# Kernel optimization log

Hardware: AMD Instinct MI355X
Metric: run time of the kernel (lower is better)

## Reference

```python
import jax, jax.numpy as jnp
import numpy as np

CS = 64          # chunk_size
CP = CS - 1      # causal_padding
H = 8            # heads
DH = 64          # dim_head
SCALE = DH ** -0.5


def rotate_half(x):
    x1, x2 = jnp.split(x, 2, axis=-1)
    return jnp.concatenate((-x2, x1), axis=-1)


def apply_rope(t, freqs):
    rd = freqs.shape[-1]
    t_rot, t_pass = t[..., :rd], t[..., rd:]
    t_rot = t_rot * jnp.cos(freqs) + rotate_half(t_rot) * jnp.sin(freqs)
    return jnp.concatenate((t_rot, t_pass), axis=-1)


def setup_inputs() -> dict:
    key = jax.random.key(0)
    ks = jax.random.split(key, 10)
    b, n, dim = 4, 4096, 1024
    k_chunks, r, rlen = 64, 2, 128
    inner = H * DH
    return {
        "x": jax.random.normal(ks[0], (b, n, dim), dtype=jnp.float32),
        "context": jax.random.normal(ks[1], (b, k_chunks, r, rlen, dim), dtype=jnp.float32),
        "q_pos_emb": jax.random.normal(ks[2], (1, 1, CS, DH), dtype=jnp.float32),
        "k_pos_emb": jax.random.normal(ks[3], (1, 1, rlen, DH), dtype=jnp.float32),
        "Wq": jax.random.normal(ks[4], (dim, inner), dtype=jnp.float32) * 0.02,
        "Wk": jax.random.normal(ks[5], (dim, inner), dtype=jnp.float32) * 0.02,
        "Wv": jax.random.normal(ks[6], (dim, inner), dtype=jnp.float32) * 0.02,
        "Wo": jax.random.normal(ks[7], (inner, dim), dtype=jnp.float32) * 0.02,
        "bo": jnp.zeros((dim,), dtype=jnp.float32),
        "null_k": jax.random.normal(ks[8], (inner,), dtype=jnp.float32),
        "null_v": jax.random.normal(ks[9], (inner,), dtype=jnp.float32),
    }


def reference(x, context, q_pos_emb, k_pos_emb, Wq, Wk, Wv, Wo, bo, null_k, null_v):
    b, n, dim = x.shape
    _, k_chunks, r, rlen, _ = context.shape
    # causal shift: drop first CP tokens, pad CP zeros at end (F.pad with -CP)
    xs = jnp.pad(x[:, CP:], ((0, 0), (0, CP), (0, 0)))
    seq_index = (n // CS) * CS
    rem = n - seq_index
    xs = xs[:, :seq_index]                                   # [b, k*CS, dim]
    # shift q rope the same way; pad region gets freqs=0 -> identity rotation
    qpe = jnp.pad(q_pos_emb[:, :, CP:], ((0, 0), (0, 0), (0, CP), (0, 0)))
    kpe = jnp.tile(k_pos_emb, (1, 1, r, 1))                  # [1,1,r*rlen,DH]
    bk = b * k_chunks
    xc = xs.reshape(bk, CS, dim)
    ctx = context.reshape(bk, r * rlen, dim)
    # projections -> [bk, h, seq, dh]
    q = (xc @ Wq).reshape(bk, CS, H, DH).transpose(0, 2, 1, 3) * SCALE
    k = (ctx @ Wk).reshape(bk, r * rlen, H, DH).transpose(0, 2, 1, 3)
    v = (ctx @ Wv).reshape(bk, r * rlen, H, DH).transpose(0, 2, 1, 3)
    q = apply_rope(q, qpe)
    k = apply_rope(k, kpe)
    # null kv prepend
    nk = jnp.broadcast_to(null_k.reshape(1, H, 1, DH), (bk, H, 1, DH))
    nv = jnp.broadcast_to(null_v.reshape(1, H, 1, DH), (bk, H, 1, DH))
    k = jnp.concatenate((nk, k), axis=2)
    v = jnp.concatenate((nv, v), axis=2)
    sim = jnp.einsum('bhid,bhjd->bhij', q, k)
    attn = jax.nn.softmax(sim, axis=-1)
    o = jnp.einsum('bhij,bhjd->bhid', attn, v)
    o = o.transpose(0, 2, 1, 3).reshape(bk, CS, H * DH)
    o = o @ Wo + bo                                          # [bk, CS, dim]
    o = o.reshape(b, k_chunks * CS, dim)
    # unshift: pad CP zeros at front, trim CP - rem from end
    o = jnp.concatenate(
        (jnp.zeros((b, CP, dim), o.dtype), o[:, :k_chunks * CS - CP + rem]), axis=1)
    return o
```

## Files before the change

### kernel.cpp

```cpp
#include <hip/hip_runtime.h>


#define DEV __device__ __forceinline__

typedef __bf16 bf16x8 __attribute__((ext_vector_type(8)));
typedef float f32x4 __attribute__((ext_vector_type(4)));

DEV unsigned short f2bf(float f) {
  union { float f; unsigned int u; } v; v.f = f;
  unsigned int u = v.u;
  unsigned int r = (u + 0x7FFFu + ((u >> 16) & 1u)) >> 16;
  return (unsigned short)r;
}
DEV float bf2f(unsigned short h) {
  union { unsigned int u; float f; } v; v.u = ((unsigned int)h) << 16;
  return v.f;
}
DEV unsigned int pkbf(unsigned int hi, unsigned int lo) {
  return __builtin_amdgcn_perm(hi, lo, 0x07060302u);
}

DEV void ldst16(const void* g, void* l) {
  __builtin_amdgcn_global_load_lds(
      (const __attribute__((address_space(1))) void*)g,
      (__attribute__((address_space(3))) void*)l, 16, 0, 0);
}

DEV void bar() { __builtin_amdgcn_s_barrier(); }
#define LGKM0 asm volatile("s_waitcnt lgkmcnt(0)" ::: "memory")
#define VMCNT4 asm volatile("s_waitcnt vmcnt(4)" ::: "memory")
#define VMCNT0 asm volatile("s_waitcnt vmcnt(0)" ::: "memory")

__global__ __launch_bounds__(256) void prep_k(const float* __restrict__ Wq,
                                              const float* __restrict__ Wk,
                                              const float* __restrict__ Wv,
                                              const float* __restrict__ Wo,
                                              const float* __restrict__ qpe,
                                              const float* __restrict__ kpe,
                                              unsigned short* __restrict__ Wqt,
                                              unsigned short* __restrict__ Wkt,
                                              unsigned short* __restrict__ Wvt,
                                              unsigned short* __restrict__ Wot,
                                              float* __restrict__ ck, float* __restrict__ sk,
                                              float* __restrict__ cq, float* __restrict__ sq,
                                              float* __restrict__ out) {
  __shared__ float tl[64][65];
  int blk = blockIdx.x;
  int tid = threadIdx.x;
  if (blk < 512) {
    int mat = blk >> 7, loc = blk & 127;
    const float* W;
    unsigned short* Wt;
    int R, C;
    float scale = 1.0f;
    if (mat == 0)      { W = Wq; Wt = Wqt; R = 1024; C = 512; scale = 0.125f; }
    else if (mat == 1) { W = Wk; Wt = Wkt; R = 1024; C = 512; }
    else if (mat == 2) { W = Wv; Wt = Wvt; R = 1024; C = 512; }
    else               { W = Wo; Wt = Wot; R = 512;  C = 1024; }
    int nct = C >> 6;
    int rt = loc / nct, ct = loc % nct;
    int r0 = rt << 6, c0 = ct << 6;
    #pragma unroll
    for (int i = 0; i < 16; ++i) {
      int flat = i * 256 + tid;
      int rr = flat >> 6, cc = flat & 63;
      tl[rr][cc] = W[(size_t)(r0 + rr) * C + c0 + cc] * scale;
    }
    __syncthreads();
    #pragma unroll
    for (int i = 0; i < 16; ++i) {
      int flat = i * 256 + tid;
      int cc = flat >> 6, rr = flat & 63;
      Wt[(size_t)(c0 + cc) * R + r0 + rr] = f2bf(tl[rr][cc]);
    }
  } else if (blk < 764) {
    int r = blk - 512;
    int b = r / 63, rr = r % 63;
    float4 z = {0.f, 0.f, 0.f, 0.f};
    *(float4*)(out + (((size_t)(b * 4096 + rr)) << 10) + tid * 4) = z;
  } else {
    int t = (blk - 764) * 256 + tid;
    float f = kpe[t];
    ck[t] = cosf(f);
    sk[t] = sinf(f);
    if (t < 64) {
      float g = qpe[63 * 64 + t];
      cq[t] = cosf(g);
      sq[t] = sinf(g);
    }
  }
}

template <int MODE>
__global__ __launch_bounds__(256) void gemm_proj(const float* __restrict__ Af,
                                                 const unsigned short* __restrict__ B0,
                                                 const unsigned short* __restrict__ B1,
                                                 unsigned short* __restrict__ out0,
                                                 unsigned short* __restrict__ out1,
                                                 const float* __restrict__ ck,
                                                 const float* __restrict__ sk,
                                                 const float* __restrict__ cq,
                                                 const float* __restrict__ sq) {
  __shared__ unsigned short sh[16384];
  unsigned short* As = sh;
  unsigned short* Bs = sh + 8192;
  const int K = 1024;

  int id = blockIdx.x;
  int x, y, z;
  if (MODE == 0) { x = (id & 7) + 8 * (id >> 5); y = (id >> 3) & 3; z = 0; }
  else           { x = (id & 7) + 8 * (id >> 6); int j = (id >> 3) & 7; y = j & 3; z = j >> 2; }
  const unsigned short* B = z ? B1 : B0;
  int m0 = x * 128, n0 = y * 128;
  int tid = threadIdx.x, w = tid >> 6, lane = tid & 63;
  int wm = (w & 1) * 64, wn = (w >> 1) * 64;
  int Lrow = lane >> 3, Lc = lane & 7;
  int srcC = Lc ^ (Lrow & 7);

  const float* asrc[4];
  bool avalid[4];
  #pragma unroll
  for (int q = 0; q < 4; ++q) {
    int t = w * 4 + q;
    int gm = m0 + t * 8 + Lrow;
    if (MODE == 0) {
      int b = gm >> 12, p = gm & 4095;
      avalid[q] = (p <= 4032);
      asrc[q] = Af + (((size_t)(b << 12) + p + 63) << 10) + srcC * 8;
    } else {
      avalid[q] = true;
      asrc[q] = Af + (size_t)gm * 1024 + srcC * 8;
    }
  }

  f32x4 acc[4][4] = {};

  for (int k0 = 0; k0 < K; k0 += 64) {
    #pragma unroll
    for (int q = 0; q < 4; ++q) {
      int t = w * 4 + q;
      uint4 lo = {0, 0, 0, 0}, hi = {0, 0, 0, 0};
      if (avalid[q]) {
        lo = *(const uint4*)(asrc[q] + k0);
        hi = *(const uint4*)(asrc[q] + k0 + 4);
      }
      uint4 pk;
      pk.x = pkbf(lo.y, lo.x);
      pk.y = pkbf(lo.w, lo.z);
      pk.z = pkbf(hi.y, hi.x);
      pk.w = pkbf(hi.w, hi.z);
      *(uint4*)((char*)As + t * 1024 + lane * 16) = pk;
      ldst16(B + (size_t)(n0 + t * 8 + Lrow) * K + (k0 + srcC * 8), (char*)Bs + t * 1024);
    }
    __syncthreads();
    #pragma unroll
    for (int k32 = 0; k32 < 2; ++k32) {
      int c = k32 * 4 + (lane >> 4);
      bf16x8 af[4], bfr[4];
      #pragma unroll
      for (int mt = 0; mt < 4; ++mt) {
        int m = wm + mt * 16 + (lane & 15);
        af[mt] = *(const bf16x8*)((const char*)As + m * 128 + (c ^ (m & 7)) * 16);
      }
      #pragma unroll
      for (int nt = 0; nt < 4; ++nt) {
        int n = wn + nt * 16 + (lane & 15);
        bfr[nt] = *(const bf16x8*)((const char*)Bs + n * 128 + (c ^ (n & 7)) * 16);
      }
      #pragma unroll
      for (int mt = 0; mt < 4; ++mt)
        #pragma unroll
        for (int nt = 0; nt < 4; ++nt)
          acc[mt][nt] = __builtin_amdgcn_mfma_f32_16x16x32_bf16(af[mt], bfr[nt], acc[mt][nt], 0, 0, 0);
    }
    __syncthreads();
  }

  if (MODE == 0) {
    #pragma unroll
    for (int mt = 0; mt < 4; ++mt)
      #pragma unroll
      for (int nt = 0; nt < 4; ++nt)
        #pragma unroll
        for (int r = 0; r < 4; ++r) {
          int m = m0 + wm + mt * 16 + (lane >> 4) * 4 + r;
          int n = n0 + wn + nt * 16 + (lane & 15);
          float val = acc[mt][nt][r];
          if ((m & 63) == 0) {
            int d = nt * 16 + (lane & 15);
            float partner = acc[mt][nt ^ 2][r];
            val = val * cq[d] + (nt < 2 ? -partner : partner) * sq[d];
          }
          out0[(size_t)m * 512 + n] = f2bf(val);
        }
  } else if (z == 0) {
    #pragma unroll
    for (int mt = 0; mt < 4; ++mt)
      #pragma unroll
      for (int r = 0; r < 4; ++r) {
        int m = m0 + wm + mt * 16 + (lane >> 4) * 4 + r;
        int fib = (m & 127) * 64;
        #pragma unroll
        for (int nt = 0; nt < 4; ++nt) {
          int n = n0 + wn + nt * 16 + (lane & 15);
          int d = nt * 16 + (lane & 15);
          float partner = acc[mt][nt ^ 2][r];
          float val = acc[mt][nt][r] * ck[fib + d] + (nt < 2 ? -partner : partner) * sk[fib + d];
          out0[(size_t)m * 512 + n] = f2bf(val);
        }
      }
  } else {
    #pragma unroll
    for (int mt = 0; mt < 4; ++mt)
      #pragma unroll
      for (int nt = 0; nt < 4; ++nt)
        #pragma unroll
        for (int r = 0; r < 4; ++r) {
          int ml = wm + mt * 16 + (lane >> 4) * 4 + r;
          int nl = wn + nt * 16 + (lane & 15);
          int mc = ml >> 3, me = ml & 7;
          *(unsigned short*)((char*)sh + nl * 256 + ((mc ^ (nl & 15)) * 16) + me * 2) =
              f2bf(acc[mt][nt][r]);
        }
    __syncthreads();
    #pragma unroll
    for (int i = 0; i < 8; ++i) {
      int flat = i * 256 + tid;
      int nl = flat >> 4, mc = flat & 15;
      uint4 v = *(const uint4*)((const char*)sh + nl * 256 + ((mc ^ (nl & 15)) * 16));
      *(uint4*)(out1 + (size_t)(n0 + nl) * 65536 + m0 + mc * 8) = v;
    }
  }
}

DEV bf16x8 rdfrag(const unsigned short* b, int row, int c) {
  return *(const bf16x8*)((const char*)b + row * 128 + ((c ^ (row & 7)) << 4));
}

DEV void rdA(const unsigned short* bufA, int wm, int ln15, int l4, int mtb,
             bf16x8 (&af)[2][2]) {
  #pragma unroll
  for (int mq = 0; mq < 2; ++mq)
    #pragma unroll
    for (int kk = 0; kk < 2; ++kk)
      af[mq][kk] = rdfrag(bufA, wm + (mtb + mq) * 16 + ln15, kk * 4 + l4);
}

DEV void rdB(const unsigned short* bufB, int wn, int ln15, int l4, bf16x8 (&bf)[4][2]) {
  #pragma unroll
  for (int nt = 0; nt < 4; ++nt)
    #pragma unroll
    for (int kk = 0; kk < 2; ++kk)
      bf[nt][kk] = rdfrag(bufB, wn + nt * 16 + ln15, kk * 4 + l4);
}

template <int MTB>
DEV void mfma16(const bf16x8 (&af)[2][2], const bf16x8 (&bf)[4][2], f32x4 (&acc)[8][4]) {
  __builtin_amdgcn_s_setprio(1);
  #pragma unroll
  for (int mq = 0; mq < 2; ++mq)
    #pragma unroll
    for (int nt = 0; nt < 4; ++nt)
      #pragma unroll
      for (int kk = 0; kk < 2; ++kk)
        acc[MTB + mq][nt] = __builtin_amdgcn_mfma_f32_16x16x32_bf16(
            af[mq][kk], bf[nt][kk], acc[MTB + mq][nt], 0, 0, 0);
  __builtin_amdgcn_s_setprio(0);
}

DEV void aload(const float* Af, int m0, int rowt, int csrc, int k0, uint4 (&al)[8]) {
  #pragma unroll
  for (int q = 0; q < 4; ++q) {
    const float* s = Af + (size_t)(m0 + q * 64 + rowt) * 1024 + k0 + csrc * 8;
    al[2 * q] = *(const uint4*)s;
    al[2 * q + 1] = *(const uint4*)(s + 4);
  }
}

DEV void apack(unsigned short* bufA, int tid, const uint4 (&al)[8]) {
  #pragma unroll
  for (int q = 0; q < 4; ++q) {
    uint4 pk;
    pk.x = pkbf(al[2 * q].y, al[2 * q].x);
    pk.y = pkbf(al[2 * q].w, al[2 * q].z);
    pk.z = pkbf(al[2 * q + 1].y, al[2 * q + 1].x);
    pk.w = pkbf(al[2 * q + 1].w, al[2 * q + 1].z);
    *(uint4*)((char*)bufA + ((q * 512 + tid) << 4)) = pk;
  }
}

DEV void bstage(unsigned short* bufB, const unsigned short* Bsrc, int n0, int w,
                int Lrow, int srcC, int k0, int h) {
  #pragma unroll
  for (int qq = 0; qq < 2; ++qq) {
    int q = 2 * h + qq;
    ldst16(Bsrc + (size_t)(n0 + q * 64 + w * 8 + Lrow) * 1024 + k0 + srcC * 8,
           (char*)bufB + ((q * 512 + w * 64) << 4));
  }
}

__global__ __launch_bounds__(512, 2) void gemm_kv(const float* __restrict__ Af,
                                                  const unsigned short* __restrict__ Bk,
                                                  const unsigned short* __restrict__ Bv,
                                                  unsigned short* __restrict__ kb,
                                                  unsigned short* __restrict__ vtg,
                                                  const float* __restrict__ ck,
                                                  const float* __restrict__ sk) {
  __shared__ unsigned short sh[65536];
  unsigned short* A0b = sh;
  unsigned short* A1b = sh + 16384;
  unsigned short* B0b = sh + 32768;
  unsigned short* B1b = sh + 49152;

  int id = blockIdx.x;
  int x = (id & 7) + 8 * (id >> 5);
  int j = (id >> 3) & 3;
  int y = j & 1, z = j >> 1;
  const unsigned short* Bz = z ? Bv : Bk;
  int m0 = x << 8, n0 = y << 8;

  int tid = threadIdx.x, w = tid >> 6, lane = tid & 63;
  int wm = (w & 1) * 128, wn = (w >> 1) * 64;
  int ln15 = lane & 15, l4 = lane >> 4;
  int Lrow = lane >> 3;
  int srcC = (lane & 7) ^ (Lrow & 7);
  int rowt = tid >> 3;
  int csrc = (tid & 7) ^ (rowt & 7);

  f32x4 acc[8][4] = {};
  uint4 al[8];

  aload(Af, m0, rowt, csrc, 0, al);
  bstage(B0b, Bz, n0, w, Lrow, srcC, 0, 0);
  bstage(B0b, Bz, n0, w, Lrow, srcC, 0, 1);
  bstage(B1b, Bz, n0, w, Lrow, srcC, 64, 0);
  bstage(B1b, Bz, n0, w, Lrow, srcC, 64, 1);
  apack(A0b, tid, al);
  LGKM0;
  VMCNT4;
  bar();

  for (int it = 0; it < 8; ++it) {
    const int k0a = it * 128;
    bf16x8 af[2][2], bf[4][2];

    rdB(B0b, wn, ln15, l4, bf);
    rdA(A0b, wm, ln15, l4, 0, af);
    aload(Af, m0, rowt, csrc, k0a + 64, al);
    bar();
    mfma16<0>(af, bf, acc);
    bar();

    rdA(A0b, wm, ln15, l4, 2, af);
    bar();
    mfma16<2>(af, bf, acc);
    bar();

    rdA(A0b, wm, ln15, l4, 4, af);
    bstage(B0b, Bz, n0, w, Lrow, srcC, (k0a + 128) & 1023, 0);
    bar();
    mfma16<4>(af, bf, acc);
    bar();

    rdA(A0b, wm, ln15, l4, 6, af);
    bstage(B0b, Bz, n0, w, Lrow, srcC, (k0a + 128) & 1023, 1);
    apack(A1b, tid, al);
    LGKM0;
    VMCNT4;
    bar();
    mfma16<6>(af, bf, acc);
    bar();

    rdB(B1b, wn, ln15, l4, bf);
    rdA(A1b, wm, ln15, l4, 0, af);
    aload(Af, m0, rowt, csrc, (k0a + 128) & 1023, al);
    bar();
    mfma16<0>(af, bf, acc);
    bar();

    rdA(A1b, wm, ln15, l4, 2, af);
    bar();
    mfma16<2>(af, bf, acc);
    bar();

    rdA(A1b, wm, ln15, l4, 4, af);
    bstage(B1b, Bz, n0, w, Lrow, srcC, (k0a + 192) & 1023, 0);
    bar();
    mfma16<4>(af, bf, acc);
    bar();

    rdA(A1b, wm, ln15, l4, 6, af);
    bstage(B1b, Bz, n0, w, Lrow, srcC, (k0a + 192) & 1023, 1);
    apack(A0b, tid, al);
    LGKM0;
    VMCNT4;
    bar();
    mfma16<6>(af, bf, acc);
    bar();
  }

  VMCNT0;
  bar();

  if (z == 0) {
    #pragma unroll
    for (int mt = 0; mt < 8; ++mt)
      #pragma unroll
      for (int r = 0; r < 4; ++r) {
        int m = m0 + wm + mt * 16 + l4 * 4 + r;
        int fib = (m & 127) << 6;
        #pragma unroll
        for (int nt = 0; nt < 4; ++nt) {
          int d = nt * 16 + ln15;
          float partner = acc[mt][nt ^ 2][r];
          float val = acc[mt][nt][r] * ck[fib + d] + (nt < 2 ? -partner : partner) * sk[fib + d];
          kb[(size_t)m * 512 + n0 + wn + d] = f2bf(val);
        }
      }
  } else {
    #pragma unroll
    for (int mt = 0; mt < 8; ++mt)
      #pragma unroll
      for (int nt = 0; nt < 4; ++nt)
        #pragma unroll
        for (int r = 0; r < 4; ++r) {
          int ml = wm + mt * 16 + l4 * 4 + r;
          int nl = wn + nt * 16 + ln15;
          int mc = ml >> 3, me = ml & 7;
          *(unsigned short*)((char*)sh + nl * 512 + ((mc ^ (nl & 31)) << 4) + me * 2) =
              f2bf(acc[mt][nt][r]);
        }
    __syncthreads();
    #pragma unroll
    for (int i = 0; i < 16; ++i) {
      int flat = i * 512 + tid;
      int nl = flat >> 5, mc = flat & 31;
      uint4 v = *(const uint4*)((const char*)sh + nl * 512 + ((mc ^ (nl & 31)) << 4));
      *(uint4*)(vtg + (size_t)(n0 + nl) * 65536 + m0 + mc * 8) = v;
    }
  }
}

__global__ __launch_bounds__(256) void gemm_out(const unsigned short* __restrict__ A,
                                                const unsigned short* __restrict__ B,
                                                const float* __restrict__ bias,
                                                float* __restrict__ out) {
  __shared__ unsigned short sh[16384];
  unsigned short* As = sh;
  unsigned short* Bs = sh + 8192;
  const int K = 512, N = 1024;
  int id = blockIdx.x;
  int x = (id & 7) + 8 * (id >> 6), y = (id >> 3) & 7;
  int m0 = x * 128, n0 = y * 128;
  int tid = threadIdx.x, w = tid >> 6, lane = tid & 63;
  int wm = (w & 1) * 64, wn = (w >> 1) * 64;
  int Lrow = lane >> 3, Lc = lane & 7;
  int srcC = Lc ^ (Lrow & 7);

  f32x4 acc[4][4] = {};

  for (int k0 = 0; k0 < K; k0 += 64) {
    #pragma unroll
    for (int q = 0; q < 4; ++q) {
      int t = w * 4 + q;
      ldst16(A + (size_t)(m0 + t * 8 + Lrow) * K + (k0 + srcC * 8), (char*)As + t * 1024);
      ldst16(B + (size_t)(n0 + t * 8 + Lrow) * K + (k0 + srcC * 8), (char*)Bs + t * 1024);
    }
    __syncthreads();
    #pragma unroll
    for (int k32 = 0; k32 < 2; ++k32) {
      int c = k32 * 4 + (lane >> 4);
      bf16x8 af[4], bfr[4];
      #pragma unroll
      for (int mt = 0; mt < 4; ++mt) {
        int m = wm + mt * 16 + (lane & 15);
        af[mt] = *(const bf16x8*)((const char*)As + m * 128 + (c ^ (m & 7)) * 16);
      }
      #pragma unroll
      for (int nt = 0; nt < 4; ++nt) {
        int n = wn + nt * 16 + (lane & 15);
        bfr[nt] = *(const bf16x8*)((const char*)Bs + n * 128 + (c ^ (n & 7)) * 16);
      }
      #pragma unroll
      for (int mt = 0; mt < 4; ++mt)
        #pragma unroll
        for (int nt = 0; nt < 4; ++nt)
          acc[mt][nt] = __builtin_amdgcn_mfma_f32_16x16x32_bf16(af[mt], bfr[nt], acc[mt][nt], 0, 0, 0);
    }
    __syncthreads();
  }
  #pragma unroll
  for (int mt = 0; mt < 4; ++mt)
    #pragma unroll
    for (int nt = 0; nt < 4; ++nt)
      #pragma unroll
      for (int r = 0; r < 4; ++r) {
        int m = m0 + wm + mt * 16 + (lane >> 4) * 4 + r;
        int n = n0 + wn + nt * 16 + (lane & 15);
        int b = m >> 12, t = m & 4095;
        if (t <= 4032)
          out[((size_t)((b << 12) + t + 63)) * N + n] = acc[mt][nt][r] + bias[n];
      }
}

__global__ __launch_bounds__(256) void attn_kernel(const unsigned short* __restrict__ qb,
                                                   const unsigned short* __restrict__ kb,
                                                   const unsigned short* __restrict__ vtg,
                                                   const float* __restrict__ nullk,
                                                   const float* __restrict__ nullv,
                                                   unsigned short* __restrict__ ob) {
  __shared__ unsigned short qs[64 * 64];
  __shared__ unsigned short ks[256 * 64];
  __shared__ unsigned short ps[64 * 256];
  __shared__ float rnull[64];
  __shared__ float rsum[64];
  int id = blockIdx.x;
  int bc = (id & 7) + 8 * (id >> 6);
  int h = (id >> 3) & 7;
  int tid = threadIdx.x, w = tid >> 6, lane = tid & 63;
  int Lrow = lane >> 3, Lc = lane & 7, srcC = Lc ^ (Lrow & 7);

  #pragma unroll
  for (int q8 = 0; q8 < 2; ++q8) {
    int t = w * 2 + q8;
    ldst16(qb + (size_t)(bc * 64 + t * 8 + Lrow) * 512 + h * 64 + srcC * 8, (char*)qs + t * 1024);
  }
  #pragma unroll
  for (int q8 = 0; q8 < 8; ++q8) {
    int t = w * 8 + q8;
    ldst16(kb + (size_t)(bc * 256 + t * 8 + Lrow) * 512 + h * 64 + srcC * 8, (char*)ks + t * 1024);
  }
  __syncthreads();

  {
    int rl = lane >> 2, part = lane & 3;
    int row = w * 16 + rl;
    float s = 0.f;
    #pragma unroll
    for (int e = 0; e < 16; ++e) {
      int d = part * 16 + e;
      unsigned short qv = *(const unsigned short*)((const char*)qs + row * 128 +
                                                   (((d >> 3) ^ (row & 7)) * 16) + (d & 7) * 2);
      s += bf2f(qv) * nullk[h * 64 + d];
    }
    s += __shfl_xor(s, 1);
    s += __shfl_xor(s, 2);
    if (part == 0) rnull[row] = __expf(s);
  }

  f32x4 acc[16] = {};
  #pragma unroll
  for (int k32 = 0; k32 < 2; ++k32) {
    int c = k32 * 4 + (lane >> 4);
    int m = w * 16 + (lane & 15);
    bf16x8 a = *(const bf16x8*)((const char*)qs + m * 128 + (c ^ (m & 7)) * 16);
    #pragma unroll
    for (int nt = 0; nt < 16; ++nt) {
      int n = nt * 16 + (lane & 15);
      bf16x8 b = *(const bf16x8*)((const char*)ks + n * 128 + (c ^ (n & 7)) * 16);
      acc[nt] = __builtin_amdgcn_mfma_f32_16x16x32_bf16(a, b, acc[nt], 0, 0, 0);
    }
  }

  int g = lane >> 4;
  #pragma unroll
  for (int r = 0; r < 4; ++r) {
    int row = w * 16 + g * 4 + r;
    float s = 0.f;
    #pragma unroll
    for (int nt = 0; nt < 16; ++nt) {
      float p = __expf(acc[nt][r]);
      acc[nt][r] = p;
      s += p;
    }
    s += __shfl_xor(s, 1);
    s += __shfl_xor(s, 2);
    s += __shfl_xor(s, 4);
    s += __shfl_xor(s, 8);
    if ((lane & 15) == 0) rsum[row] = s + rnull[row];
  }

  #pragma unroll
  for (int nt = 0; nt < 16; ++nt)
    #pragma unroll
    for (int r = 0; r < 4; ++r) {
      int row = w * 16 + g * 4 + r;
      int col = nt * 16 + (lane & 15);
      *(unsigned short*)((char*)ps + row * 512 + (((col >> 3) ^ (row & 7)) * 16) + (col & 7) * 2) =
          f2bf(acc[nt][r]);
    }
  __syncthreads();

  #pragma unroll
  for (int q8 = 0; q8 < 8; ++q8) {
    int t = w * 8 + q8;
    int dd = t * 2 + (lane >> 5);
    int cl = (lane & 31) ^ (dd & 7);
    ldst16(vtg + (size_t)(h * 64 + dd) * 65536 + bc * 256 + cl * 8, (char*)ks + t * 1024);
  }
  __syncthreads();

  f32x4 oacc[4] = {};
  #pragma unroll
  for (int k32 = 0; k32 < 8; ++k32) {
    int c = k32 * 4 + (lane >> 4);
    int m = w * 16 + (lane & 15);
    bf16x8 a = *(const bf16x8*)((const char*)ps + m * 512 + (c ^ (m & 7)) * 16);
    #pragma unroll
    for (int nt = 0; nt < 4; ++nt) {
      int n = nt * 16 + (lane & 15);
      bf16x8 b = *(const bf16x8*)((const char*)ks + n * 512 + (c ^ (n & 7)) * 16);
      oacc[nt] = __builtin_amdgcn_mfma_f32_16x16x32_bf16(a, b, oacc[nt], 0, 0, 0);
    }
  }
  #pragma unroll
  for (int nt = 0; nt < 4; ++nt)
    #pragma unroll
    for (int r = 0; r < 4; ++r) {
      int row = w * 16 + g * 4 + r;
      int d = nt * 16 + (lane & 15);
      float o = oacc[nt][r] + rnull[row] * nullv[h * 64 + d];
      o /= rsum[row];
      ob[((size_t)(bc * 64 + row) * 8 + h) * 64 + d] = f2bf(o);
    }
}

extern "C" void kernel_launch(void* const* d_in, const int* in_sizes, int n_in,
                              void* d_out, int out_size, void* d_ws, size_t ws_size,
                              hipStream_t stream) {
  const float* x = (const float*)d_in[0];
  const float* ctx = (const float*)d_in[1];
  const float* qpe = (const float*)d_in[2];
  const float* kpe = (const float*)d_in[3];
  const float* Wq = (const float*)d_in[4];
  const float* Wk = (const float*)d_in[5];
  const float* Wv = (const float*)d_in[6];
  const float* Wo = (const float*)d_in[7];
  const float* bo = (const float*)d_in[8];
  const float* nk = (const float*)d_in[9];
  const float* nv = (const float*)d_in[10];
  float* out = (float*)d_out;
  char* ws = (char*)d_ws;

  unsigned short* Wqt  = (unsigned short*)(ws + 0);
  unsigned short* Wkt  = (unsigned short*)(ws + 1048576);
  unsigned short* Wvt  = (unsigned short*)(ws + 2097152);
  unsigned short* Wot  = (unsigned short*)(ws + 3145728);
  unsigned short* qb   = (unsigned short*)(ws + 4194304);
  unsigned short* kb   = (unsigned short*)(ws + 20971520);
  unsigned short* vtg  = (unsigned short*)(ws + 88080384);
  unsigned short* obuf = (unsigned short*)(ws + 155189248);
  float* cosk = (float*)(ws + 171966464);
  float* sink = (float*)(ws + 171999232);
  float* cosq = (float*)(ws + 172032000);
  float* sinq = (float*)(ws + 172032256);

  prep_k<<<796, 256, 0, stream>>>(Wq, Wk, Wv, Wo, qpe, kpe, Wqt, Wkt, Wvt, Wot,
                                  cosk, sink, cosq, sinq, out);

  gemm_proj<0><<<512, 256, 0, stream>>>(x, Wqt, Wqt, qb, nullptr,
                                        cosk, sink, cosq, sinq);
  gemm_kv<<<1024, 512, 0, stream>>>(ctx, Wkt, Wvt, kb, vtg, cosk, sink);

  attn_kernel<<<2048, 256, 0, stream>>>(qb, kb, vtg, nk, nv, obuf);

  gemm_out<<<1024, 256, 0, stream>>>(obuf, Wot, bo, out);
}
```

Baseline: 707.2 us.

## Pre-cast context to bf16 in halves and stage A via direct LDS loads

Result: no change. 708.5 us (+0.2%).

```diff
diff --git a/kernel.cpp b/kernel.cpp
--- a/kernel.cpp
+++ b/kernel.cpp
@@ -27,7 +27,6 @@
 }
 
 DEV void bar() { __builtin_amdgcn_s_barrier(); }
-#define LGKM0 asm volatile("s_waitcnt lgkmcnt(0)" ::: "memory")
 #define VMCNT4 asm volatile("s_waitcnt vmcnt(4)" ::: "memory")
 #define VMCNT0 asm volatile("s_waitcnt vmcnt(0)" ::: "memory")
 
@@ -91,6 +90,19 @@
   }
 }
 
+__global__ __launch_bounds__(256) void cast_k(const float* __restrict__ src,
+                                              unsigned short* __restrict__ dst) {
+  size_t base = ((size_t)blockIdx.x * 256 + threadIdx.x) * 8;
+  uint4 lo = *(const uint4*)(src + base);
+  uint4 hi = *(const uint4*)(src + base + 4);
+  uint4 pk;
+  pk.x = pkbf(lo.y, lo.x);
+  pk.y = pkbf(lo.w, lo.z);
+  pk.z = pkbf(hi.y, hi.x);
+  pk.w = pkbf(hi.w, hi.z);
+  *(uint4*)(dst + base) = pk;
+}
+
 template <int MODE>
 __global__ __launch_bounds__(256) void gemm_proj(const float* __restrict__ Af,
                                                  const unsigned short* __restrict__ B0,
@@ -268,44 +280,24 @@
   __builtin_amdgcn_s_setprio(0);
 }
 
-DEV void aload(const float* Af, int m0, int rowt, int csrc, int k0, uint4 (&al)[8]) {
-  #pragma unroll
-  for (int q = 0; q < 4; ++q) {
-    const float* s = Af + (size_t)(m0 + q * 64 + rowt) * 1024 + k0 + csrc * 8;
-    al[2 * q] = *(const uint4*)s;
-    al[2 * q + 1] = *(const uint4*)(s + 4);
-  }
-}
-
-DEV void apack(unsigned short* bufA, int tid, const uint4 (&al)[8]) {
-  #pragma unroll
-  for (int q = 0; q < 4; ++q) {
-    uint4 pk;
-    pk.x = pkbf(al[2 * q].y, al[2 * q].x);
-    pk.y = pkbf(al[2 * q].w, al[2 * q].z);
-    pk.z = pkbf(al[2 * q + 1].y, al[2 * q + 1].x);
-    pk.w = pkbf(al[2 * q + 1].w, al[2 * q + 1].z);
-    *(uint4*)((char*)bufA + ((q * 512 + tid) << 4)) = pk;
-  }
-}
-
-DEV void bstage(unsigned short* bufB, const unsigned short* Bsrc, int n0, int w,
-                int Lrow, int srcC, int k0, int h) {
+DEV void stg(unsigned short* buf, const unsigned short* src, int r0, int w,
+             int Lrow, int srcC, int k0, int h) {
   #pragma unroll
   for (int qq = 0; qq < 2; ++qq) {
     int q = 2 * h + qq;
-    ldst16(Bsrc + (size_t)(n0 + q * 64 + w * 8 + Lrow) * 1024 + k0 + srcC * 8,
-           (char*)bufB + ((q * 512 + w * 64) << 4));
-  }
-}
-
-__global__ __launch_bounds__(512, 2) void gemm_kv(const float* __restrict__ Af,
+    ldst16(src + (size_t)(r0 + q * 64 + w * 8 + Lrow) * 1024 + (k0 + srcC * 8),
+           (char*)buf + ((q * 512 + w * 64) << 4));
+  }
+}
+
+__global__ __launch_bounds__(512, 2) void gemm_kv(const unsigned short* __restrict__ Abf,
                                                   const unsigned short* __restrict__ Bk,
                                                   const unsigned short* __restrict__ Bv,
                                                   unsigned short* __restrict__ kb,
                                                   unsigned short* __restrict__ vtg,
                                                   const float* __restrict__ ck,
-                                                  const float* __restrict__ sk) {
+                                                  const float* __restrict__ sk,
+                                                  int mbase) {
   __shared__ unsigned short sh[65536];
   unsigned short* A0b = sh;
   unsigned short* A1b = sh + 16384;
@@ -317,86 +309,66 @@
   int j = (id >> 3) & 3;
   int y = j & 1, z = j >> 1;
   const unsigned short* Bz = z ? Bv : Bk;
-  int m0 = x << 8, n0 = y << 8;
+  int m0l = x << 8;
+  int m0 = mbase + m0l;
+  int n0 = y << 8;
 
   int tid = threadIdx.x, w = tid >> 6, lane = tid & 63;
   int wm = (w & 1) * 128, wn = (w >> 1) * 64;
   int ln15 = lane & 15, l4 = lane >> 4;
   int Lrow = lane >> 3;
   int srcC = (lane & 7) ^ (Lrow & 7);
-  int rowt = tid >> 3;
-  int csrc = (tid & 7) ^ (rowt & 7);
 
   f32x4 acc[8][4] = {};
-  uint4 al[8];
-
-  aload(Af, m0, rowt, csrc, 0, al);
-  bstage(B0b, Bz, n0, w, Lrow, srcC, 0, 0);
-  bstage(B0b, Bz, n0, w, Lrow, srcC, 0, 1);
-  bstage(B1b, Bz, n0, w, Lrow, srcC, 64, 0);
-  bstage(B1b, Bz, n0, w, Lrow, srcC, 64, 1);
-  apack(A0b, tid, al);
-  LGKM0;
+
+  stg(A0b, Abf, m0l, w, Lrow, srcC, 0, 0);
+  stg(A0b, Abf, m0l, w, Lrow, srcC, 0, 1);
+  stg(B0b, Bz, n0, w, Lrow, srcC, 0, 0);
+  stg(B0b, Bz, n0, w, Lrow, srcC, 0, 1);
+  stg(B1b, Bz, n0, w, Lrow, srcC, 64, 0);
+  stg(B1b, Bz, n0, w, Lrow, srcC, 64, 1);
   VMCNT4;
   bar();
 
   for (int it = 0; it < 8; ++it) {
-    const int k0a = it * 128;
+    const int k0 = it * 128;
     bf16x8 af[2][2], bf[4][2];
 
     rdB(B0b, wn, ln15, l4, bf);
     rdA(A0b, wm, ln15, l4, 0, af);
-    aload(Af, m0, rowt, csrc, k0a + 64, al);
-    bar();
-    mfma16<0>(af, bf, acc);
-    bar();
+    stg(A1b, Abf, m0l, w, Lrow, srcC, k0 + 64, 0);
+    bar(); mfma16<0>(af, bf, acc); bar();
 
     rdA(A0b, wm, ln15, l4, 2, af);
-    bar();
-    mfma16<2>(af, bf, acc);
-    bar();
+    stg(A1b, Abf, m0l, w, Lrow, srcC, k0 + 64, 1);
+    bar(); mfma16<2>(af, bf, acc); bar();
 
     rdA(A0b, wm, ln15, l4, 4, af);
-    bstage(B0b, Bz, n0, w, Lrow, srcC, (k0a + 128) & 1023, 0);
-    bar();
-    mfma16<4>(af, bf, acc);
-    bar();
+    stg(B0b, Bz, n0, w, Lrow, srcC, (k0 + 128) & 1023, 0);
+    bar(); mfma16<4>(af, bf, acc); bar();
 
     rdA(A0b, wm, ln15, l4, 6, af);
-    bstage(B0b, Bz, n0, w, Lrow, srcC, (k0a + 128) & 1023, 1);
-    apack(A1b, tid, al);
-    LGKM0;
+    stg(B0b, Bz, n0, w, Lrow, srcC, (k0 + 128) & 1023, 1);
     VMCNT4;
-    bar();
-    mfma16<6>(af, bf, acc);
-    bar();
+    bar(); mfma16<6>(af, bf, acc); bar();
 
     rdB(B1b, wn, ln15, l4, bf);
     rdA(A1b, wm, ln15, l4, 0, af);
-    aload(Af, m0, rowt, csrc, (k0a + 128) & 1023, al);
-    bar();
-    mfma16<0>(af, bf, acc);
-    bar();
+    stg(A0b, Abf, m0l, w, Lrow, srcC, (k0 + 128) & 1023, 0);
+    bar(); mfma16<0>(af, bf, acc); bar();
 
     rdA(A1b, wm, ln15, l4, 2, af);
-    bar();
-    mfma16<2>(af, bf, acc);
-    bar();
+    stg(A0b, Abf, m0l, w, Lrow, srcC, (k0 + 128) & 1023, 1);
+    bar(); mfma16<2>(af, bf, acc); bar();
 
     rdA(A1b, wm, ln15, l4, 4, af);
-    bstage(B1b, Bz, n0, w, Lrow, srcC, (k0a + 192) & 1023, 0);
-    bar();
-    mfma16<4>(af, bf, acc);
-    bar();
+    stg(B1b, Bz, n0, w, Lrow, srcC, (k0 + 192) & 1023, 0);
+    bar(); mfma16<4>(af, bf, acc); bar();
 
     rdA(A1b, wm, ln15, l4, 6, af);
-    bstage(B1b, Bz, n0, w, Lrow, srcC, (k0a + 192) & 1023, 1);
-    apack(A0b, tid, al);
-    LGKM0;
+    stg(B1b, Bz, n0, w, Lrow, srcC, (k0 + 192) & 1023, 1);
     VMCNT4;
-    bar();
-    mfma16<6>(af, bf, acc);
-    bar();
+    bar(); mfma16<6>(af, bf, acc); bar();
   }
 
   VMCNT0;
@@ -646,21 +618,26 @@
   unsigned short* Wkt  = (unsigned short*)(ws + 1048576);
   unsigned short* Wvt  = (unsigned short*)(ws + 2097152);
   unsigned short* Wot  = (unsigned short*)(ws + 3145728);
-  unsigned short* qb   = (unsigned short*)(ws + 4194304);
-  unsigned short* kb   = (unsigned short*)(ws + 20971520);
-  unsigned short* vtg  = (unsigned short*)(ws + 88080384);
-  unsigned short* obuf = (unsigned short*)(ws + 155189248);
-  float* cosk = (float*)(ws + 171966464);
-  float* sink = (float*)(ws + 171999232);
-  float* cosq = (float*)(ws + 172032000);
-  float* sinq = (float*)(ws + 172032256);
+  float* cosk = (float*)(ws + 4194304);
+  float* sink = (float*)(ws + 4227072);
+  float* cosq = (float*)(ws + 4259840);
+  float* sinq = (float*)(ws + 4260096);
+  unsigned short* qb   = (unsigned short*)(ws + 4260352);
+  unsigned short* kb   = (unsigned short*)(ws + 21037568);
+  unsigned short* vtg  = (unsigned short*)(ws + 88146432);
+  unsigned short* obuf = (unsigned short*)(ws + 155255296);
+  unsigned short* ctxb = (unsigned short*)(ws + 155255296);
 
   prep_k<<<796, 256, 0, stream>>>(Wq, Wk, Wv, Wo, qpe, kpe, Wqt, Wkt, Wvt, Wot,
                                   cosk, sink, cosq, sinq, out);
 
   gemm_proj<0><<<512, 256, 0, stream>>>(x, Wqt, Wqt, qb, nullptr,
                                         cosk, sink, cosq, sinq);
-  gemm_kv<<<1024, 512, 0, stream>>>(ctx, Wkt, Wvt, kb, vtg, cosk, sink);
+
+  cast_k<<<16384, 256, 0, stream>>>(ctx, ctxb);
+  gemm_kv<<<512, 512, 0, stream>>>(ctxb, Wkt, Wvt, kb, vtg, cosk, sink, 0);
+  cast_k<<<16384, 256, 0, stream>>>(ctx + 33554432, ctxb);
+  gemm_kv<<<512, 512, 0, stream>>>(ctxb, Wkt, Wvt, kb, vtg, cosk, sink, 32768);
 
   attn_kernel<<<2048, 256, 0, stream>>>(qb, kb, vtg, nk, nv, obuf);
 
```
